# Kernel optimization log

Measured on AMD Instinct MI355X. Metric: run time of the kernel, lower is better.

Reference implementation:

```python
import jax, jax.numpy as jnp
import numpy as np

D_MODEL = 512
N_EXPERTS = 8
TOPK = 2
D_FF = D_MODEL * 4
LB_WEIGHT = 0.01


def setup_inputs() -> dict:
    key = jax.random.key(0)
    k_x, k_g, k_w1, k_v1, k_w2 = jax.random.split(key, 5)
    B, L = 4, 2048
    x = jax.random.normal(k_x, (B, L, D_MODEL), dtype=jnp.float32)
    # nn.Linear gate weight, init std=0.01, shape [n_experts, d_model]
    gate_w = 0.01 * jax.random.normal(k_g, (N_EXPERTS, D_MODEL), dtype=jnp.float32)
    # kaiming_normal_ fan_in / relu: std = sqrt(2 / fan_in); fan_in is last dim
    std1 = np.sqrt(2.0 / D_MODEL).astype(np.float32)
    std2 = np.sqrt(2.0 / D_FF).astype(np.float32)
    W1 = std1 * jax.random.normal(k_w1, (N_EXPERTS, D_FF, D_MODEL), dtype=jnp.float32)
    V1 = std1 * jax.random.normal(k_v1, (N_EXPERTS, D_FF, D_MODEL), dtype=jnp.float32)
    W2 = std2 * jax.random.normal(k_w2, (N_EXPERTS, D_MODEL, D_FF), dtype=jnp.float32)
    return {"x": x, "gate_w": gate_w, "W1": W1, "V1": V1, "W2": W2}


def reference(x, gate_w, W1, V1, W2):
    B, L, D = x.shape
    T = B * L
    x_flat = x.reshape(T, D)

    # --- gating ---
    logits = x_flat @ gate_w.T                      # [T, E]
    probs = jax.nn.softmax(logits, axis=-1)         # [T, E]
    scores, indices = jax.lax.top_k(probs, TOPK)    # [T, K] each

    # combine weights: [T, E]; top-k indices per token are distinct
    oh = jax.nn.one_hot(indices, N_EXPERTS, dtype=x.dtype)    # [T, K, E]
    combine = jnp.einsum('tke,tk->te', oh, scores)            # [T, E]

    # load-balancing aux loss
    load = oh.sum(axis=(0, 1))                      # [E] tokens routed per expert
    f = load / T
    P = probs.mean(axis=0)                          # [E]
    aux_loss = N_EXPERTS * jnp.sum(f * P) * LB_WEIGHT

    # --- SwiGLU experts (dense over experts, masked combine) ---
    h = jnp.einsum('td,efd->etf', x_flat, W1)       # [E, T, d_ff]
    v = jnp.einsum('td,efd->etf', x_flat, V1)       # [E, T, d_ff]
    y = jnp.einsum('etf,edf->etd', jax.nn.silu(h) * v, W2)   # [E, T, D]

    out = jnp.einsum('te,etd->td', combine, y).reshape(B, L, D)
    return out, aux_loss
```

## Files before the change

### kernel.cpp

```cpp
#include <hip/hip_runtime.h>
#include <hip/hip_bf16.h>
#include <stdint.h>

#define D_MODEL 512
#define N_EXP 8
#define D_FF 2048
#define NTOK 8192
#define TM 256
#define MAX_TILES 72
#define NEPAD (MAX_TILES*TM)
#define BK 64

typedef __attribute__((ext_vector_type(8))) short short8;
typedef __attribute__((ext_vector_type(4))) float f32x4;

struct Ctrl {
  int cnt[8];
  int cursor[8];
  int offpad[16];
  int ntiles;
  int pad[3];
  int texp[MAX_TILES];
};

__device__ __forceinline__ unsigned short f2bf(float f){
  unsigned u = __float_as_uint(f);
  u += 0x7FFFu + ((u>>16)&1u);
  return (unsigned short)(u>>16);
}
__device__ __forceinline__ float bf2f(unsigned short v){
  return __uint_as_float(((unsigned)v)<<16);
}

__device__ __forceinline__ short8 pack8(float4 a, float4 b){
  short8 o;
  o[0]=(short)f2bf(a.x); o[1]=(short)f2bf(a.y); o[2]=(short)f2bf(a.z); o[3]=(short)f2bf(a.w);
  o[4]=(short)f2bf(b.x); o[5]=(short)f2bf(b.y); o[6]=(short)f2bf(b.z); o[7]=(short)f2bf(b.w);
  return o;
}

__device__ __forceinline__ void gload16(const void* g, void* l){
  __builtin_amdgcn_global_load_lds((const __attribute__((address_space(1))) unsigned int*)g,
                                   (__attribute__((address_space(3))) unsigned int*)l, 16, 0, 0);
}

#define SBAR0 __builtin_amdgcn_sched_barrier(0)
#define BAR   do{ SBAR0; __builtin_amdgcn_s_barrier(); SBAR0; }while(0)
#define LGKM0 do{ asm volatile("s_waitcnt lgkmcnt(0)" ::: "memory"); SBAR0; }while(0)
#define VM0   do{ asm volatile("s_waitcnt vmcnt(0)" ::: "memory"); SBAR0; }while(0)

__global__ void __launch_bounds__(256)
cvt3_kernel(const float* __restrict__ s0, const float* __restrict__ s1, const float* __restrict__ s2,
            unsigned short* __restrict__ d0, unsigned short* __restrict__ d1, unsigned short* __restrict__ d2){
  const float* src = (blockIdx.y==0) ? s0 : (blockIdx.y==1 ? s1 : s2);
  unsigned short* dst = (blockIdx.y==0) ? d0 : (blockIdx.y==1 ? d1 : d2);
  int i = (blockIdx.x*256 + threadIdx.x)*8;
  float4 a = *(const float4*)(src+i);
  float4 b = *(const float4*)(src+i+4);
  *(short8*)(dst+i) = pack8(a,b);
}

__global__ void __launch_bounds__(256)
cvt_kernel(const float* __restrict__ src, unsigned short* __restrict__ dst, int n){
  int i = (blockIdx.x*256 + threadIdx.x)*8;
  if(i >= n) return;
  float4 a = *(const float4*)(src+i);
  float4 b = *(const float4*)(src+i+4);
  *(short8*)(dst+i) = pack8(a,b);
}

__global__ void __launch_bounds__(256)
gate_kernel(const float* __restrict__ x, const float* __restrict__ gw,
            int* __restrict__ tok_e, float* __restrict__ tok_s,
            Ctrl* __restrict__ c, float* __restrict__ Ppart,
            unsigned short* __restrict__ Xb){
  __shared__ float gws[N_EXP*D_MODEL];
  __shared__ float pblk[4][8];
  __shared__ int cblk[8];
  int tid = threadIdx.x;
  for(int i=tid; i<N_EXP*D_MODEL; i+=256) gws[i]=gw[i];
  if(tid<8) cblk[tid]=0;
  __syncthreads();
  int wave = tid>>6, lane = tid&63;
  int t = blockIdx.x*4 + wave;
  const float* xr = x + (size_t)t*D_MODEL + lane*8;
  float4 xa = *(const float4*)xr;
  float4 xb = *(const float4*)(xr+4);
  *(short8*)(Xb + (size_t)t*D_MODEL + lane*8) = pack8(xa,xb);
  float le[8];
  #pragma unroll
  for(int e=0;e<8;e++){
    const float* g = gws + e*D_MODEL + lane*8;
    float4 ga = *(const float4*)g;
    float4 gb = *(const float4*)(g+4);
    le[e] = xa.x*ga.x + xa.y*ga.y + xa.z*ga.z + xa.w*ga.w
          + xb.x*gb.x + xb.y*gb.y + xb.z*gb.z + xb.w*gb.w;
  }
  #pragma unroll
  for(int e=0;e<8;e++){
    float v = le[e];
    #pragma unroll
    for(int off=1; off<64; off<<=1) v += __shfl_xor(v, off);
    le[e]=v;
  }
  float mx = le[0];
  #pragma unroll
  for(int e=1;e<8;e++) mx = fmaxf(mx, le[e]);
  float p[8], s=0.f;
  #pragma unroll
  for(int e=0;e<8;e++){ p[e]=__expf(le[e]-mx); s+=p[e]; }
  float inv = 1.0f/s;
  #pragma unroll
  for(int e=0;e<8;e++) p[e]*=inv;
  int e0=0; float s0=p[0];
  #pragma unroll
  for(int e=1;e<8;e++) if(p[e]>s0){e0=e;s0=p[e];}
  int e1=-1; float s1=-1.f;
  #pragma unroll
  for(int e=0;e<8;e++) if(e!=e0 && p[e]>s1){e1=e;s1=p[e];}
  if(lane==0){
    tok_e[2*t]=e0; tok_e[2*t+1]=e1;
    tok_s[2*t]=s0; tok_s[2*t+1]=s1;
    atomicAdd(&cblk[e0],1); atomicAdd(&cblk[e1],1);
    #pragma unroll
    for(int e=0;e<8;e++) pblk[wave][e]=p[e];
  }
  __syncthreads();
  if(tid<8){
    atomicAdd(&c->cnt[tid], cblk[tid]);
    Ppart[blockIdx.x*8+tid] = pblk[0][tid]+pblk[1][tid]+pblk[2][tid]+pblk[3][tid];
  }
}

__global__ void __launch_bounds__(256)
scan_kernel(Ctrl* __restrict__ c, const float* __restrict__ Ppart, float* __restrict__ out){
  __shared__ float red[256];
  __shared__ float tot[8];
  int tid = threadIdx.x;
  for(int e=0;e<8;e++){
    float v=0.f;
    for(int i=tid;i<2048;i+=256) v += Ppart[i*8+e];
    red[tid]=v; __syncthreads();
    for(int s=128;s>0;s>>=1){ if(tid<s) red[tid]+=red[tid+s]; __syncthreads(); }
    if(tid==0) tot[e]=red[0];
    __syncthreads();
  }
  if(tid==0){
    int o=0, tc=0;
    float aux=0.f;
    for(int e=0;e<8;e++){
      c->offpad[e]=o;
      int nt = (c->cnt[e]+TM-1)/TM;
      for(int i=0;i<nt;i++) c->texp[tc++]=e;
      o += nt*TM;
      c->cursor[e]=0;
      aux += ((float)c->cnt[e]/(float)NTOK) * (tot[e]/(float)NTOK);
    }
    c->offpad[8]=o;
    c->ntiles=tc;
    out[(size_t)NTOK*D_MODEL] = 8.0f*0.01f*aux;
  }
}

__global__ void __launch_bounds__(256)
scatter_kernel(const int* __restrict__ tok_e, const float* __restrict__ tok_s,
               Ctrl* __restrict__ c, int* __restrict__ etok, float* __restrict__ escl,
               int* __restrict__ pos){
  int t = blockIdx.x*256 + threadIdx.x;
  if(t >= NTOK) return;
  #pragma unroll
  for(int k=0;k<2;k++){
    int e = tok_e[2*t+k];
    int p = atomicAdd(&c->cursor[e],1);
    int i = c->offpad[e]+p;
    etok[i]=t; escl[i]=tok_s[2*t+k];
    pos[2*t+k]=i;
  }
}

__global__ void __launch_bounds__(256,2)
expA_kernel(const unsigned short* __restrict__ Xb, const unsigned short* __restrict__ W1b,
            const unsigned short* __restrict__ V1b, const int* __restrict__ etok,
            const Ctrl* __restrict__ c, unsigned short* __restrict__ G){
  __shared__ short8 As[2][1024];
  __shared__ short8 Bs[2][1024];
  int bid = blockIdx.x;
  int chunk = bid & 7;
  int w = bid >> 3;
  int fb = w / 18;
  int mtile = chunk*18 + (w - fb*18);
  if(mtile >= (c->offpad[8] >> 7)) return;
  int e = c->texp[mtile>>1];
  int base = mtile*128;
  int fbase = fb*64;
  int tid = threadIdx.x;

  int r0 = tid>>3, cc = tid&7;
  int cs = cc ^ (r0&7);
  const unsigned short* sA0; const unsigned short* sA1;
  const unsigned short* sA2; const unsigned short* sA3;
  { int tok;
    tok = etok[base + r0      ]; sA0 = Xb + (size_t)tok*D_MODEL + cs*8;
    tok = etok[base + r0 + 32 ]; sA1 = Xb + (size_t)tok*D_MODEL + cs*8;
    tok = etok[base + r0 + 64 ]; sA2 = Xb + (size_t)tok*D_MODEL + cs*8;
    tok = etok[base + r0 + 96 ]; sA3 = Xb + (size_t)tok*D_MODEL + cs*8;
  }
  const unsigned short* WE = W1b + (size_t)e*(D_FF*D_MODEL);
  const unsigned short* VE = V1b + (size_t)e*(D_FF*D_MODEL);
  const unsigned short* sW0 = WE + (size_t)(fbase + r0     )*D_MODEL + cs*8;
  const unsigned short* sW1 = WE + (size_t)(fbase + r0 + 32)*D_MODEL + cs*8;
  const unsigned short* sV0 = VE + (size_t)(fbase + r0     )*D_MODEL + cs*8;
  const unsigned short* sV1 = VE + (size_t)(fbase + r0 + 32)*D_MODEL + cs*8;
  int w64 = tid & ~63;

  int lane = tid&63, lrow = lane&15, lk = lane>>4;
  int wv = tid>>6, wm = wv>>1, wf = wv&1;

  f32x4 hacc[4][2], vacc[4][2];
  #pragma unroll
  for(int mi=0;mi<4;mi++)
    #pragma unroll
    for(int fj=0;fj<2;fj++){
      hacc[mi][fj]=(f32x4){0.f,0.f,0.f,0.f};
      vacc[mi][fj]=(f32x4){0.f,0.f,0.f,0.f};
    }

  auto STAGE = [&](int b, int t){
    size_t o = (size_t)t*BK;
    gload16(sA0+o, &As[b][w64      ]);
    gload16(sA1+o, &As[b][w64 + 256]);
    gload16(sA2+o, &As[b][w64 + 512]);
    gload16(sA3+o, &As[b][w64 + 768]);
    gload16(sW0+o, &Bs[b][w64      ]);
    gload16(sW1+o, &Bs[b][w64 + 256]);
    gload16(sV0+o, &Bs[b][w64 + 512]);
    gload16(sV1+o, &Bs[b][w64 + 768]);
  };

  STAGE(0,0);
  VM0; BAR;

  #pragma unroll
  for(int t=0;t<8;t++){
    const int cur = t&1;
    if(t<7) STAGE(cur^1, t+1);
    short8 a[4][2], bw[2][2], bv[2][2];
    #pragma unroll
    for(int ks=0;ks<2;ks++){
      #pragma unroll
      for(int mi=0;mi<4;mi++){
        int arow = wm*64 + mi*16 + lrow;
        a[mi][ks] = As[cur][arow*8 + ((ks*4+lk) ^ (arow&7))];
      }
      #pragma unroll
      for(int fj=0;fj<2;fj++){
        int wrow = wf*32 + fj*16 + lrow;
        int sl = wrow*8 + ((ks*4+lk) ^ (wrow&7));
        bw[fj][ks] = Bs[cur][sl];
        bv[fj][ks] = Bs[cur][512 + sl];
      }
    }
    LGKM0;
    __builtin_amdgcn_s_setprio(1);
    #pragma unroll
    for(int ks=0;ks<2;ks++)
      #pragma unroll
      for(int mi=0;mi<4;mi++)
        #pragma unroll
        for(int fj=0;fj<2;fj++){
          hacc[mi][fj] = __builtin_amdgcn_mfma_f32_16x16x32_bf16(a[mi][ks], bw[fj][ks], hacc[mi][fj],0,0,0);
          vacc[mi][fj] = __builtin_amdgcn_mfma_f32_16x16x32_bf16(a[mi][ks], bv[fj][ks], vacc[mi][fj],0,0,0);
        }
    __builtin_amdgcn_s_setprio(0);
    VM0; BAR;
  }

  #pragma unroll
  for(int mi=0;mi<4;mi++){
    #pragma unroll
    for(int fj=0;fj<2;fj++){
      int f = fbase + wf*32 + fj*16 + lrow;
      #pragma unroll
      for(int r=0;r<4;r++){
        int m = base + wm*64 + mi*16 + lk*4 + r;
        float h = hacc[mi][fj][r], vv = vacc[mi][fj][r];
        float g = (h/(1.0f+__expf(-h)))*vv;
        G[(size_t)m*D_FF + f] = f2bf(g);
      }
    }
  }
}

__global__ void __launch_bounds__(256,2)
expB_kernel(const unsigned short* __restrict__ G, const unsigned short* __restrict__ W2b,
            const Ctrl* __restrict__ c, unsigned short* __restrict__ Ye){
  __shared__ short8 As2[2][1024];
  __shared__ short8 Bs2[2][1024];
  int bid = blockIdx.x;
  int chunk = bid & 7;
  int w = bid >> 3;
  int nb = w / 18;
  int mtile = chunk*18 + (w - nb*18);
  if(mtile >= (c->offpad[8] >> 7)) return;
  int e = c->texp[mtile>>1];
  int base = mtile*128;
  int nbase = nb*128;
  int tid = threadIdx.x;

  int r0 = tid>>3, cc = tid&7;
  int cs = cc ^ (r0&7);
  const unsigned short* sA0 = G + (size_t)(base + r0     )*D_FF + cs*8;
  const unsigned short* sA1 = G + (size_t)(base + r0 + 32)*D_FF + cs*8;
  const unsigned short* sA2 = G + (size_t)(base + r0 + 64)*D_FF + cs*8;
  const unsigned short* sA3 = G + (size_t)(base + r0 + 96)*D_FF + cs*8;
  const unsigned short* W2E = W2b + (size_t)e*(D_MODEL*D_FF);
  const unsigned short* sB0 = W2E + (size_t)(nbase + r0     )*D_FF + cs*8;
  const unsigned short* sB1 = W2E + (size_t)(nbase + r0 + 32)*D_FF + cs*8;
  const unsigned short* sB2 = W2E + (size_t)(nbase + r0 + 64)*D_FF + cs*8;
  const unsigned short* sB3 = W2E + (size_t)(nbase + r0 + 96)*D_FF + cs*8;
  int w64 = tid & ~63;

  int lane = tid&63, lrow = lane&15, lk = lane>>4;
  int wv = tid>>6, wm = wv>>1, wn = wv&1;

  f32x4 acc[4][4];
  #pragma unroll
  for(int mi=0;mi<4;mi++)
    #pragma unroll
    for(int nj=0;nj<4;nj++) acc[mi][nj]=(f32x4){0.f,0.f,0.f,0.f};

  auto STAGE = [&](int b, int t){
    size_t o = (size_t)t*BK;
    gload16(sA0+o, &As2[b][w64      ]);
    gload16(sA1+o, &As2[b][w64 + 256]);
    gload16(sA2+o, &As2[b][w64 + 512]);
    gload16(sA3+o, &As2[b][w64 + 768]);
    gload16(sB0+o, &Bs2[b][w64      ]);
    gload16(sB1+o, &Bs2[b][w64 + 256]);
    gload16(sB2+o, &Bs2[b][w64 + 512]);
    gload16(sB3+o, &Bs2[b][w64 + 768]);
  };

  STAGE(0,0);
  VM0; BAR;

  #pragma unroll 2
  for(int t=0;t<32;t++){
    const int cur = t&1;
    if(t<31) STAGE(cur^1, t+1);
    short8 a[4][2], b[4][2];
    #pragma unroll
    for(int ks=0;ks<2;ks++){
      #pragma unroll
      for(int mi=0;mi<4;mi++){
        int arow = wm*64 + mi*16 + lrow;
        a[mi][ks] = As2[cur][arow*8 + ((ks*4+lk) ^ (arow&7))];
      }
      #pragma unroll
      for(int nj=0;nj<4;nj++){
        int brow = wn*64 + nj*16 + lrow;
        b[nj][ks] = Bs2[cur][brow*8 + ((ks*4+lk) ^ (brow&7))];
      }
    }
    LGKM0;
    __builtin_amdgcn_s_setprio(1);
    #pragma unroll
    for(int ks=0;ks<2;ks++)
      #pragma unroll
      for(int mi=0;mi<4;mi++)
        #pragma unroll
        for(int nj=0;nj<4;nj++)
          acc[mi][nj] = __builtin_amdgcn_mfma_f32_16x16x32_bf16(a[mi][ks], b[nj][ks], acc[mi][nj],0,0,0);
    __builtin_amdgcn_s_setprio(0);
    VM0; BAR;
  }

  #pragma unroll
  for(int mi=0;mi<4;mi++){
    #pragma unroll
    for(int r=0;r<4;r++){
      int m = base + wm*64 + mi*16 + lk*4 + r;
      #pragma unroll
      for(int nj=0;nj<4;nj++){
        int n = nbase + wn*64 + nj*16 + lrow;
        Ye[(size_t)m*D_MODEL + n] = f2bf(acc[mi][nj][r]);
      }
    }
  }
}

__global__ void __launch_bounds__(256)
combine_kernel(const unsigned short* __restrict__ Ye, const int* __restrict__ pos,
               const float* __restrict__ tok_s, float* __restrict__ out){
  int wave = threadIdx.x>>6, lane = threadIdx.x&63;
  int t = blockIdx.x*4 + wave;
  int p0 = pos[2*t], p1 = pos[2*t+1];
  float s0 = tok_s[2*t], s1 = tok_s[2*t+1];
  short8 y0 = *(const short8*)(Ye + (size_t)p0*D_MODEL + lane*8);
  short8 y1 = *(const short8*)(Ye + (size_t)p1*D_MODEL + lane*8);
  float* o = out + (size_t)t*D_MODEL + lane*8;
  float v[8];
  #pragma unroll
  for(int i=0;i<8;i++)
    v[i] = s0*bf2f((unsigned short)y0[i]) + s1*bf2f((unsigned short)y1[i]);
  float4 lo = {v[0],v[1],v[2],v[3]};
  float4 hi = {v[4],v[5],v[6],v[7]};
  *(float4*)o = lo;
  *(float4*)(o+4) = hi;
}

extern "C" void kernel_launch(void* const* d_in, const int* in_sizes, int n_in,
                              void* d_out, int out_size, void* d_ws, size_t ws_size,
                              hipStream_t stream) {
  (void)in_sizes; (void)n_in; (void)out_size;
  const float* x  = (const float*)d_in[0];
  const float* gw = (const float*)d_in[1];
  const float* W1 = (const float*)d_in[2];
  const float* V1 = (const float*)d_in[3];
  const float* W2 = (const float*)d_in[4];
  float* out = (float*)d_out;

  const size_t WSZ = (size_t)N_EXP*D_FF*D_MODEL;
  const size_t XSZ = (size_t)NTOK*D_MODEL;
  char* ws = (char*)d_ws;
  size_t off = 0;
  unsigned short* W1b = (unsigned short*)(ws+off); off += WSZ*2;
  unsigned short* V1b = (unsigned short*)(ws+off); size_t v1_off = off; off += WSZ*2;
  unsigned short* Xb  = (unsigned short*)(ws+off); off += XSZ*2;
  unsigned short* G   = (unsigned short*)(ws+off); off += (size_t)NEPAD*D_FF*2;
  int*   etok  = (int*)(ws+off);   size_t entry_off = off; off += (size_t)NEPAD*4;
  float* escl  = (float*)(ws+off); off += (size_t)NEPAD*4;
  size_t entry_bytes = off - entry_off;
  int*   pos   = (int*)(ws+off);   off += (size_t)NTOK*2*4;
  int*   tok_e = (int*)(ws+off);   off += (size_t)NTOK*2*4;
  float* tok_s = (float*)(ws+off); off += (size_t)NTOK*2*4;
  float* Ppart = (float*)(ws+off); off += (size_t)2048*8*4;
  Ctrl*  ctrl  = (Ctrl*)(ws+off);  off += sizeof(Ctrl);
  unsigned short* Ye  = (unsigned short*)(ws+v1_off);
  if(ws_size < off) return;

  unsigned short* W2d = (unsigned short*)(ws+off);
  bool hoistW2 = (ws_size >= off + WSZ*2);
  unsigned short* W2b = hoistW2 ? W2d : W1b;

  hipMemsetAsync(ws+entry_off, 0, entry_bytes, stream);
  hipMemsetAsync(ctrl, 0, sizeof(Ctrl), stream);

  cvt3_kernel<<<dim3(4096, hoistW2 ? 3 : 2), 256, 0, stream>>>(W1, V1, W2, W1b, V1b, W2d);

  gate_kernel<<<NTOK/4, 256, 0, stream>>>(x, gw, tok_e, tok_s, ctrl, Ppart, Xb);
  scan_kernel<<<1, 256, 0, stream>>>(ctrl, Ppart, out);
  scatter_kernel<<<NTOK/256, 256, 0, stream>>>(tok_e, tok_s, ctrl, etok, escl, pos);

  expA_kernel<<<4608, 256, 0, stream>>>(Xb, W1b, V1b, etok, ctrl, G);
  if(!hoistW2)
    cvt_kernel<<<(int)WSZ/(256*8), 256, 0, stream>>>(W2, W1b, (int)WSZ);
  expB_kernel<<<576, 256, 0, stream>>>(G, W2b, ctrl, Ye);
  combine_kernel<<<NTOK/4, 256, 0, stream>>>(Ye, pos, tok_s, out);
}
```

Baseline: 346.4 us.

## Enlarge expA tiles to 256x128 with 512 threads and pipeline waits

Restructures the gate/up expert GEMM so each 512-thread block computes a 256-token by 128-ff tile with a BK of 32, cutting the grid from 4608 to 1152 blocks and raising operand reuse per staged load. It changes the LDS swizzle and interleaves LDS reads with MFMA groups. In both expert kernels the full vmcnt(0) wait after each stage becomes a partial vmcnt so the next stage's prefetch stays in flight, with barriers placed before and after. The trade-offs are more accumulator registers per thread, a smaller K step with more barriers, and fewer blocks to fill the device.

```diff
diff --git a/kernel.cpp b/kernel.cpp
--- a/kernel.cpp
+++ b/kernel.cpp
@@ -9,7 +9,6 @@
 #define TM 256
 #define MAX_TILES 72
 #define NEPAD (MAX_TILES*TM)
-#define BK 64
 
 typedef __attribute__((ext_vector_type(8))) short short8;
 typedef __attribute__((ext_vector_type(4))) float f32x4;
@@ -46,8 +45,7 @@
 
 #define SBAR0 __builtin_amdgcn_sched_barrier(0)
 #define BAR   do{ SBAR0; __builtin_amdgcn_s_barrier(); SBAR0; }while(0)
-#define LGKM0 do{ asm volatile("s_waitcnt lgkmcnt(0)" ::: "memory"); SBAR0; }while(0)
-#define VM0   do{ asm volatile("s_waitcnt vmcnt(0)" ::: "memory"); SBAR0; }while(0)
+#define VM(N) do{ asm volatile("s_waitcnt vmcnt(" #N ")" ::: "memory"); SBAR0; }while(0)
 
 __global__ void __launch_bounds__(256)
 cvt3_kernel(const float* __restrict__ s0, const float* __restrict__ s1, const float* __restrict__ s2,
@@ -178,7 +176,7 @@
   }
 }
 
-__global__ void __launch_bounds__(256,2)
+__global__ void __launch_bounds__(512,2)
 expA_kernel(const unsigned short* __restrict__ Xb, const unsigned short* __restrict__ W1b,
             const unsigned short* __restrict__ V1b, const int* __restrict__ etok,
             const Ctrl* __restrict__ c, unsigned short* __restrict__ G){
@@ -186,106 +184,103 @@
   __shared__ short8 Bs[2][1024];
   int bid = blockIdx.x;
   int chunk = bid & 7;
-  int w = bid >> 3;
-  int fb = w / 18;
-  int mtile = chunk*18 + (w - fb*18);
-  if(mtile >= (c->offpad[8] >> 7)) return;
-  int e = c->texp[mtile>>1];
-  int base = mtile*128;
-  int fbase = fb*64;
+  int w_in = bid >> 3;
+  int fb = w_in / 9;
+  int tile = chunk*9 + (w_in - fb*9);
+  int fbase = fb * 128;
+  if(tile >= c->ntiles) return;
+  int e = c->texp[tile];
+  int base = tile*TM;
   int tid = threadIdx.x;
 
-  int r0 = tid>>3, cc = tid&7;
-  int cs = cc ^ (r0&7);
-  const unsigned short* sA0; const unsigned short* sA1;
-  const unsigned short* sA2; const unsigned short* sA3;
-  { int tok;
-    tok = etok[base + r0      ]; sA0 = Xb + (size_t)tok*D_MODEL + cs*8;
-    tok = etok[base + r0 + 32 ]; sA1 = Xb + (size_t)tok*D_MODEL + cs*8;
-    tok = etok[base + r0 + 64 ]; sA2 = Xb + (size_t)tok*D_MODEL + cs*8;
-    tok = etok[base + r0 + 96 ]; sA3 = Xb + (size_t)tok*D_MODEL + cs*8;
-  }
+  int r = tid>>2, cc = tid&3;
+  int swr = (r ^ (r>>2)) & 3;
+  int cs = cc ^ swr;
+  int t0 = etok[base + r];
+  int t1 = etok[base + 128 + r];
+  const unsigned short* sA0 = Xb + (size_t)t0*D_MODEL + cs*8;
+  const unsigned short* sA1 = Xb + (size_t)t1*D_MODEL + cs*8;
   const unsigned short* WE = W1b + (size_t)e*(D_FF*D_MODEL);
   const unsigned short* VE = V1b + (size_t)e*(D_FF*D_MODEL);
-  const unsigned short* sW0 = WE + (size_t)(fbase + r0     )*D_MODEL + cs*8;
-  const unsigned short* sW1 = WE + (size_t)(fbase + r0 + 32)*D_MODEL + cs*8;
-  const unsigned short* sV0 = VE + (size_t)(fbase + r0     )*D_MODEL + cs*8;
-  const unsigned short* sV1 = VE + (size_t)(fbase + r0 + 32)*D_MODEL + cs*8;
+  const unsigned short* sB0 = WE + (size_t)(fbase+r)*D_MODEL + cs*8;
+  const unsigned short* sB1 = VE + (size_t)(fbase+r)*D_MODEL + cs*8;
   int w64 = tid & ~63;
 
   int lane = tid&63, lrow = lane&15, lk = lane>>4;
-  int wv = tid>>6, wm = wv>>1, wf = wv&1;
-
-  f32x4 hacc[4][2], vacc[4][2];
-  #pragma unroll
-  for(int mi=0;mi<4;mi++)
-    #pragma unroll
-    for(int fj=0;fj<2;fj++){
-      hacc[mi][fj]=(f32x4){0.f,0.f,0.f,0.f};
-      vacc[mi][fj]=(f32x4){0.f,0.f,0.f,0.f};
+  int wid = tid>>6, wr = wid>>2, wc = wid&3;
+  int sw = (lrow ^ (lrow>>2)) & 3;
+  int ch = lk ^ sw;
+
+  f32x4 hacc[8][2], vacc[8][2];
+  #pragma unroll
+  for(int mi=0;mi<8;mi++)
+    #pragma unroll
+    for(int nj=0;nj<2;nj++){
+      hacc[mi][nj]=(f32x4){0.f,0.f,0.f,0.f};
+      vacc[mi][nj]=(f32x4){0.f,0.f,0.f,0.f};
     }
 
-  auto STAGE = [&](int b, int t){
-    size_t o = (size_t)t*BK;
-    gload16(sA0+o, &As[b][w64      ]);
-    gload16(sA1+o, &As[b][w64 + 256]);
-    gload16(sA2+o, &As[b][w64 + 512]);
-    gload16(sA3+o, &As[b][w64 + 768]);
-    gload16(sW0+o, &Bs[b][w64      ]);
-    gload16(sW1+o, &Bs[b][w64 + 256]);
-    gload16(sV0+o, &Bs[b][w64 + 512]);
-    gload16(sV1+o, &Bs[b][w64 + 768]);
+  auto STAGE = [&](int b, int kt){
+    size_t o = (size_t)kt*32;
+    gload16(sA0+o, &As[b][w64]);
+    gload16(sA1+o, &As[b][512+w64]);
+    gload16(sB0+o, &Bs[b][w64]);
+    gload16(sB1+o, &Bs[b][512+w64]);
   };
 
   STAGE(0,0);
-  VM0; BAR;
-
-  #pragma unroll
-  for(int t=0;t<8;t++){
-    const int cur = t&1;
-    if(t<7) STAGE(cur^1, t+1);
-    short8 a[4][2], bw[2][2], bv[2][2];
-    #pragma unroll
-    for(int ks=0;ks<2;ks++){
-      #pragma unroll
-      for(int mi=0;mi<4;mi++){
-        int arow = wm*64 + mi*16 + lrow;
-        a[mi][ks] = As[cur][arow*8 + ((ks*4+lk) ^ (arow&7))];
-      }
-      #pragma unroll
-      for(int fj=0;fj<2;fj++){
-        int wrow = wf*32 + fj*16 + lrow;
-        int sl = wrow*8 + ((ks*4+lk) ^ (wrow&7));
-        bw[fj][ks] = Bs[cur][sl];
-        bv[fj][ks] = Bs[cur][512 + sl];
-      }
-    }
-    LGKM0;
+
+  #pragma unroll 2
+  for(int kt=0; kt<16; kt++){
+    const int cur = kt&1, nxt = cur^1;
+    BAR;
+    if(kt<15) STAGE(nxt, kt+1);
+    if(kt<15){ VM(4); } else { VM(0); }
+    BAR;
+    short8 alo[4], ahi[4], bw[2], bv[2];
     __builtin_amdgcn_s_setprio(1);
     #pragma unroll
-    for(int ks=0;ks<2;ks++)
-      #pragma unroll
-      for(int mi=0;mi<4;mi++)
-        #pragma unroll
-        for(int fj=0;fj<2;fj++){
-          hacc[mi][fj] = __builtin_amdgcn_mfma_f32_16x16x32_bf16(a[mi][ks], bw[fj][ks], hacc[mi][fj],0,0,0);
-          vacc[mi][fj] = __builtin_amdgcn_mfma_f32_16x16x32_bf16(a[mi][ks], bv[fj][ks], vacc[mi][fj],0,0,0);
-        }
+    for(int j=0;j<4;j++) alo[j] = As[cur][(wr*128 + j*16 + lrow)*4 + ch];
+    #pragma unroll
+    for(int nj=0;nj<2;nj++) bw[nj] = Bs[cur][(wc*32 + nj*16 + lrow)*4 + ch];
+    #pragma unroll
+    for(int j=0;j<4;j++)
+      #pragma unroll
+      for(int nj=0;nj<2;nj++)
+        hacc[j][nj] = __builtin_amdgcn_mfma_f32_16x16x32_bf16(alo[j], bw[nj], hacc[j][nj],0,0,0);
+    #pragma unroll
+    for(int nj=0;nj<2;nj++) bv[nj] = Bs[cur][512 + (wc*32 + nj*16 + lrow)*4 + ch];
+    #pragma unroll
+    for(int j=0;j<4;j++)
+      #pragma unroll
+      for(int nj=0;nj<2;nj++)
+        vacc[j][nj] = __builtin_amdgcn_mfma_f32_16x16x32_bf16(alo[j], bv[nj], vacc[j][nj],0,0,0);
+    #pragma unroll
+    for(int j=0;j<4;j++) ahi[j] = As[cur][(wr*128 + 64 + j*16 + lrow)*4 + ch];
+    #pragma unroll
+    for(int j=0;j<4;j++)
+      #pragma unroll
+      for(int nj=0;nj<2;nj++)
+        vacc[4+j][nj] = __builtin_amdgcn_mfma_f32_16x16x32_bf16(ahi[j], bv[nj], vacc[4+j][nj],0,0,0);
+    #pragma unroll
+    for(int j=0;j<4;j++)
+      #pragma unroll
+      for(int nj=0;nj<2;nj++)
+        hacc[4+j][nj] = __builtin_amdgcn_mfma_f32_16x16x32_bf16(ahi[j], bw[nj], hacc[4+j][nj],0,0,0);
     __builtin_amdgcn_s_setprio(0);
-    VM0; BAR;
-  }
-
-  #pragma unroll
-  for(int mi=0;mi<4;mi++){
-    #pragma unroll
-    for(int fj=0;fj<2;fj++){
-      int f = fbase + wf*32 + fj*16 + lrow;
-      #pragma unroll
-      for(int r=0;r<4;r++){
-        int m = base + wm*64 + mi*16 + lk*4 + r;
-        float h = hacc[mi][fj][r], vv = vacc[mi][fj][r];
+  }
+
+  #pragma unroll
+  for(int mi=0;mi<8;mi++){
+    int m = base + wr*128 + mi*16 + lk*4;
+    #pragma unroll
+    for(int nj=0;nj<2;nj++){
+      int f = fbase + wc*32 + nj*16 + lrow;
+      #pragma unroll
+      for(int rr=0;rr<4;rr++){
+        float h = hacc[mi][nj][rr], vv = vacc[mi][nj][rr];
         float g = (h/(1.0f+__expf(-h)))*vv;
-        G[(size_t)m*D_FF + f] = f2bf(g);
+        G[(size_t)(m+rr)*D_FF + f] = f2bf(g);
       }
     }
   }
@@ -330,7 +325,7 @@
     for(int nj=0;nj<4;nj++) acc[mi][nj]=(f32x4){0.f,0.f,0.f,0.f};
 
   auto STAGE = [&](int b, int t){
-    size_t o = (size_t)t*BK;
+    size_t o = (size_t)t*64;
     gload16(sA0+o, &As2[b][w64      ]);
     gload16(sA1+o, &As2[b][w64 + 256]);
     gload16(sA2+o, &As2[b][w64 + 512]);
@@ -342,12 +337,14 @@
   };
 
   STAGE(0,0);
-  VM0; BAR;
 
   #pragma unroll 2
   for(int t=0;t<32;t++){
-    const int cur = t&1;
-    if(t<31) STAGE(cur^1, t+1);
+    const int cur = t&1, nxt = cur^1;
+    BAR;
+    if(t<31) STAGE(nxt, t+1);
+    if(t<31){ VM(8); } else { VM(0); }
+    BAR;
     short8 a[4][2], b[4][2];
     #pragma unroll
     for(int ks=0;ks<2;ks++){
@@ -362,7 +359,6 @@
         b[nj][ks] = Bs2[cur][brow*8 + ((ks*4+lk) ^ (brow&7))];
       }
     }
-    LGKM0;
     __builtin_amdgcn_s_setprio(1);
     #pragma unroll
     for(int ks=0;ks<2;ks++)
@@ -372,7 +368,6 @@
         for(int nj=0;nj<4;nj++)
           acc[mi][nj] = __builtin_amdgcn_mfma_f32_16x16x32_bf16(a[mi][ks], b[nj][ks], acc[mi][nj],0,0,0);
     __builtin_amdgcn_s_setprio(0);
-    VM0; BAR;
   }
 
   #pragma unroll
@@ -452,7 +447,7 @@
   scan_kernel<<<1, 256, 0, stream>>>(ctrl, Ppart, out);
   scatter_kernel<<<NTOK/256, 256, 0, stream>>>(tok_e, tok_s, ctrl, etok, escl, pos);
 
-  expA_kernel<<<4608, 256, 0, stream>>>(Xb, W1b, V1b, etok, ctrl, G);
+  expA_kernel<<<1152, 512, 0, stream>>>(Xb, W1b, V1b, etok, ctrl, G);
   if(!hoistW2)
     cvt_kernel<<<(int)WSZ/(256*8), 256, 0, stream>>>(W2, W1b, (int)WSZ);
   expB_kernel<<<576, 256, 0, stream>>>(G, W2b, ctrl, Ye);
```

Result: slower. 357.7 us (+3.3%).
